# Optimization experiments

Hardware: AMD Instinct MI355X
Metric: run time of the kernel (lower is better)

The kernel has to match this reference:

```python
import jax, jax.numpy as jnp
import numpy as np

INFTY_APPROX = 1e30
LAM = 10000.0


def sinusoid_embs(length, width):
    # Transformer-XL sinusoidal embeddings, flipped so row 0 encodes the
    # largest relative distance (length-1), matching the rel_shift convention.
    pos = jnp.arange(length, dtype=jnp.float32)
    inv_lams = 1.0 / (LAM ** (jnp.arange(0, width, 2, dtype=jnp.float32) / width))
    pre = pos[:, None] * inv_lams[None, :]                 # [T, width//2]
    cat = jnp.concatenate([jnp.sin(pre), jnp.cos(pre)], axis=-1)  # [T, width]
    return jnp.flip(cat, axis=0)


def rel_shift(x):
    # x: [B, T, T] -> out[b,i,j] = x[b, i, j - i + T - 1] (XL pad/reshape trick)
    b, t, _ = x.shape
    x = jnp.pad(x, ((0, 0), (0, 0), (1, 0)))               # [B, T, T+1]
    x = x.reshape(b, t + 1, t)[:, 1:, :]                   # [B, T, T]
    return x


def setup_inputs() -> dict:
    B, T, D, K, V = 2, 4096, 1024, 128, 2048
    key = jax.random.key(0)
    ks = jax.random.split(key, 10)
    s_d = 1.0 / np.sqrt(D)
    s_v = 1.0 / np.sqrt(V)
    return {
        'x':    jax.random.normal(ks[0], (B, T, D), dtype=jnp.float32),
        'g_ln': jnp.ones((D,), dtype=jnp.float32),
        'W_q':  s_d * jax.random.normal(ks[1], (D, K), dtype=jnp.float32),
        'W_k':  s_d * jax.random.normal(ks[2], (D, K), dtype=jnp.float32),
        'W_v':  s_d * jax.random.normal(ks[3], (D, V), dtype=jnp.float32),
        'W_g':  s_d * jax.random.normal(ks[4], (D, V), dtype=jnp.float32),
        'W_r':  s_d * jax.random.normal(ks[5], (D, K), dtype=jnp.float32),
        'xl_u': 0.02 * jax.random.normal(ks[6], (K,), dtype=jnp.float32),
        'xl_v': 0.02 * jax.random.normal(ks[7], (K,), dtype=jnp.float32),
        'W_o':  s_v * jax.random.normal(ks[8], (V, D), dtype=jnp.float32),
    }


def reference(x, g_ln, W_q, W_k, W_v, W_g, W_r, xl_u, xl_v, W_o):
    B, T, D = x.shape
    K = W_q.shape[-1]
    tau = jnp.asarray(K, x.dtype) ** 0.5

    # RMSNorm input layernorm
    x_tilde = x * jax.lax.rsqrt(jnp.mean(jnp.square(x), axis=-1, keepdims=True) + 1e-6)
    x_tilde = x_tilde * g_ln

    # QKVG projections; queries pre-scaled by 1/tau (producer-side scaling)
    q = (x_tilde @ W_q) / tau                              # [B, T, K]
    k = x_tilde @ W_k                                      # [B, T, K]
    v = x_tilde @ W_v                                      # [B, T, V]

    # XL relative-position bias inputs
    xl_r = sinusoid_embs(T, D) @ W_r                       # [T, K]

    # AC term (content) and BD term (position) with XL u/v biases
    scores_ac = jnp.einsum('bik,bjk->bij', q + xl_u, k)    # [B, T, T]
    scores_bd = jnp.einsum('bik,jk->bij', q + xl_v, xl_r)  # [B, T, T]
    scores_bd = rel_shift(scores_bd)

    scores = scores_ac + scores_bd
    keep = jnp.tril(jnp.ones((T, T), dtype=bool))          # causal keep mask
    scores = scores - jnp.asarray(INFTY_APPROX, x.dtype) * jnp.logical_not(keep)

    w = jax.nn.softmax(scores, axis=-1)                    # [B, T, T]
    wv = jnp.einsum('bij,bjv->biv', w, v)                  # [B, T, V]

    # SHGA gating (GAU-style silu gate)
    wv = wv * jax.nn.silu(x_tilde @ W_g)

    res = wv @ W_o                                         # [B, T, D]
    return res
```

## Files before the change

kernel.cpp:

```cpp
#include <hip/hip_runtime.h>
#include <hip/hip_bf16.h>
#include <stdint.h>

typedef __attribute__((ext_vector_type(4))) float f32x4;
typedef __attribute__((ext_vector_type(8))) short s16x8;
typedef __attribute__((ext_vector_type(8))) unsigned short u16x8;
typedef __attribute__((ext_vector_type(4))) unsigned short u16x4;

static __device__ __forceinline__ float b2f(unsigned short u) {
  union { unsigned int i; float f; } v; v.i = ((unsigned int)u) << 16; return v.f;
}
static __device__ __forceinline__ unsigned short f2b(float f) {
  unsigned int x = __float_as_uint(f);
  return (unsigned short)((x + 0x7fffu + ((x >> 16) & 1u)) >> 16);
}

typedef __attribute__((address_space(1))) const void gconst_t;
typedef __attribute__((address_space(3))) void lds_t;
static __device__ __forceinline__ void gload_lds16(const void* g, void* l) {
  __builtin_amdgcn_global_load_lds((gconst_t*)g, (lds_t*)l, 16, 0, 0);
}

template<int N>
static __device__ __forceinline__ void vmwait() {
  asm volatile("s_waitcnt vmcnt(%0)" :: "n"(N) : "memory");
}
static __device__ __forceinline__ void barmid() {
  __builtin_amdgcn_sched_barrier(0);
  __builtin_amdgcn_s_barrier();
  asm volatile("s_waitcnt lgkmcnt(0)" ::: "memory");
  __builtin_amdgcn_sched_barrier(0);
}
static __device__ __forceinline__ void barend() {
  __builtin_amdgcn_sched_barrier(0);
  __builtin_amdgcn_s_barrier();
}

struct GemmP {
  const unsigned short* A; const unsigned short* B; void* C;
  long sA, sB, sC;
  int M, N, K, lda, ldb, ldc;
  int causal, kend_mode, swapxy;
  int gxs, gys, qchunk;
  const float* uvec; const float* vvec;
  unsigned short* qv_out; unsigned short* kk_out; float invtau;
  const float* rinv; const unsigned short* gate;
  const unsigned short* bds; float* stats;
};

template<int EPI>
__launch_bounds__(512, 2)
__global__ void gemm8p256_k(GemmP p) {
  __shared__ unsigned short L[2][4][8192];
  const int lin = (int)blockIdx.x + (int)gridDim.x * ((int)blockIdx.y + (int)gridDim.y * (int)blockIdx.z);
  const int wg = (lin & 7) * p.qchunk + (lin >> 3);
  const int xx = wg & ((1 << p.gxs) - 1);
  const int yy = (wg >> p.gxs) & ((1 << p.gys) - 1);
  const int ii = p.swapxy ? yy : xx;
  const int jj = p.swapxy ? xx : yy;
  const int i0 = ii * 256, j0 = jj * 256;
  const unsigned short* Ag = p.A + (long)i0 * p.lda;
  const unsigned short* Bg = p.B + (long)j0 * p.ldb;
  const int lda = p.lda, ldb = p.ldb;
  const int NI = p.K >> 7;

  const int tid = threadIdx.x;
  const int w = tid >> 6, l = tid & 63;
  const int wr = w >> 2, wc = w & 3;
  const int fr = l & 15, fq = l >> 4;

  auto stA = [&](int slot, int h, int t) {
#pragma unroll
    for (int u = 0; u < 2; ++u) {
      const int sl = u * 512 + tid, r = sl >> 3, g = sl & 7;
      const int gs = g ^ (r & 7);
      gload_lds16(Ag + (long)(h * 128 + r) * lda + t * 64 + gs * 8, &L[slot][h][sl * 8]);
    }
  };
  auto stB = [&](int slot, int h, int t) {
#pragma unroll
    for (int u = 0; u < 2; ++u) {
      const int sl = u * 512 + tid, r = sl >> 3, g = sl & 7;
      const int gs = g ^ (r & 7);
      gload_lds16(Bg + (long)(h * 128 + r) * ldb + t * 64 + gs * 8, &L[slot][2 + h][sl * 8]);
    }
  };

  f32x4 acc[8][4];
#pragma unroll
  for (int m = 0; m < 8; ++m)
#pragma unroll
    for (int n = 0; n < 4; ++n) acc[m][n] = (f32x4){0.f, 0.f, 0.f, 0.f};

  const int sx = (fr & 7) << 4;
  const int abase = ((fr << 7) + (fq << 4)) ^ sx;
  const int bbase = (((wc & 1) << 13) + (fr << 7) + (fq << 4)) ^ sx;
  s16x8 a[4][2], bA[2][2], bB[2][2];

  auto rdA = [&](int slot, int mq) {
#pragma unroll
    for (int m = 0; m < 4; ++m)
#pragma unroll
      for (int ks = 0; ks < 2; ++ks)
        a[m][ks] = *(const s16x8*)((const char*)&L[slot][wr][0] +
                                   ((abase ^ (ks << 6)) | ((mq * 4 + m) << 11)));
  };
  auto rdB = [&](int slot, int nq, s16x8 (&bb)[2][2]) {
    const int reg = 2 + (wc >> 1);
#pragma unroll
    for (int n = 0; n < 2; ++n)
#pragma unroll
      for (int ks = 0; ks < 2; ++ks)
        bb[n][ks] = *(const s16x8*)((const char*)&L[slot][reg][0] +
                                    ((bbase ^ (ks << 6)) | ((nq * 2 + n) << 11)));
  };
  auto mm = [&](int mq, int nq, s16x8 (&bb)[2][2]) {
    __builtin_amdgcn_s_setprio(1);
#pragma unroll
    for (int m = 0; m < 4; ++m)
#pragma unroll
      for (int n = 0; n < 2; ++n)
#pragma unroll
        for (int ks = 0; ks < 2; ++ks)
          acc[mq * 4 + m][nq * 2 + n] =
              __builtin_amdgcn_mfma_f32_16x16x32_bf16(a[m][ks], bb[n][ks],
                                                      acc[mq * 4 + m][nq * 2 + n], 0, 0, 0);
    __builtin_amdgcn_s_setprio(0);
  };

  stB(0, 0, 0); stB(0, 1, 0); stA(0, 0, 0); stA(0, 1, 0);
  stB(1, 0, 1); stB(1, 1, 1);
  vmwait<4>();
  barend();

  for (int it = 0; it < NI; ++it) {
    const int t0 = 2 * it, t1 = t0 + 1;
    const bool lastI = (it == NI - 1);
    rdA(0, 0); rdB(0, 0, bA); stA(1, 0, t1);
    barmid(); mm(0, 0, bA); barend();
    rdB(0, 1, bB); stA(1, 1, t1);
    barmid(); mm(0, 1, bB); barend();
    rdA(0, 1);
    if (!lastI) stB(0, 0, t0 + 2);
    barmid(); mm(1, 1, bB); barend();
    if (!lastI) stB(0, 1, t0 + 2);
    barmid(); mm(1, 0, bA);
    if (lastI) vmwait<0>(); else vmwait<4>();
    barend();
    rdA(1, 0); rdB(1, 0, bA);
    if (!lastI) stA(0, 0, t0 + 2);
    barmid(); mm(0, 0, bA); barend();
    rdB(1, 1, bB);
    if (!lastI) stA(0, 1, t0 + 2);
    barmid(); mm(0, 1, bB); barend();
    rdA(1, 1);
    if (!lastI) stB(1, 0, t1 + 2);
    barmid(); mm(1, 1, bB); barend();
    if (!lastI) stB(1, 1, t1 + 2);
    barmid(); mm(1, 0, bA);
    if (!lastI) vmwait<4>();
    barend();
  }

  const int rb = i0 + wr * 128 + fq * 4;
  const int cb = j0 + wc * 64 + fr;
#pragma unroll
  for (int m = 0; m < 8; ++m)
#pragma unroll
    for (int n = 0; n < 4; ++n) {
      const int col = cb + n * 16;
#pragma unroll
      for (int e = 0; e < 4; ++e) {
        const int row = rb + m * 16 + e;
        const float val = acc[m][n][e];
        if constexpr (EPI == 0)
          ((unsigned short*)p.C)[(long)row * p.ldc + col] = f2b(val);
        else
          ((unsigned short*)p.C)[(long)row * p.ldc + col] = f2b(val / (1.f + __expf(-val)));
      }
    }
}

template<int PAIR, int EPI>
__launch_bounds__(512, 2)
__global__ void gemm8p128_k(GemmP p) {
  __shared__ unsigned short L[3][3][8192];
  const int lin = (int)blockIdx.x + (int)gridDim.x * ((int)blockIdx.y + (int)gridDim.y * (int)blockIdx.z);
  const int wg = (lin & 7) * p.qchunk + (lin >> 3);
  const int xx = wg & ((1 << p.gxs) - 1);
  const int yy = (wg >> p.gxs) & ((1 << p.gys) - 1);
  const int b  = wg >> (p.gxs + p.gys);
  const int jj = PAIR ? yy : (p.swapxy ? xx : yy);
  const int j0 = jj * 128;
  const unsigned short* Bg0 = p.B + (long)b * p.sB + (long)j0 * p.ldb;
  const int lda = p.lda, ldb = p.ldb;

  const int tid = threadIdx.x;
  const int w = tid >> 6, l = tid & 63;
  const int wr = w >> 1, wc = w & 1;
  const int fr = l & 15, fq = l >> 4;

  const int sx = (fr & 7) << 4;
  const int abase = ((((wr & 1) << 13) + (fr << 7) + (fq << 4))) ^ sx;
  const int bbase = (((wc << 13) + (fr << 7) + (fq << 4))) ^ sx;

  const int passes = PAIR ? 2 : 1;
  for (int ps = 0; ps < passes; ++ps) {
    const int ii = PAIR ? (ps ? xx : (15 - xx)) : (p.swapxy ? yy : xx);
    const int i0 = ii * 256;
    const unsigned short* Ag = p.A + (long)b * p.sA + (long)i0 * lda;
    const int kend = p.kend_mode ? min(p.K, i0 + 256) : p.K;
    const int NT = kend >> 6;

    auto stA = [&](int slot, int h, int t) {
#pragma unroll
      for (int u = 0; u < 2; ++u) {
        const int sl = u * 512 + tid, r = sl >> 3, g = sl & 7;
        const int gs = g ^ (r & 7);
        gload_lds16(Ag + (long)(h * 128 + r) * lda + t * 64 + gs * 8, &L[slot][h][sl * 8]);
      }
    };
    auto stB = [&](int slot, int bh, int t) {
      const int r = tid >> 3, g = tid & 7;
      const int rloc = bh * 64 + r;
      const int gs = g ^ (rloc & 7);
      gload_lds16(Bg0 + (long)rloc * ldb + t * 64 + gs * 8, &L[slot][2][bh * 4096 + tid * 8]);
    };

    f32x4 acc[4][4];
#pragma unroll
    for (int m = 0; m < 4; ++m)
#pragma unroll
      for (int n = 0; n < 4; ++n) acc[m][n] = (f32x4){0.f, 0.f, 0.f, 0.f};
    s16x8 a[4][2], bA[2][2], bB[2][2];

    auto rdA = [&](int slot) {
      const int reg = wr >> 1;
#pragma unroll
      for (int m = 0; m < 4; ++m)
#pragma unroll
        for (int ks = 0; ks < 2; ++ks)
          a[m][ks] = *(const s16x8*)((const char*)&L[slot][reg][0] +
                                     ((abase ^ (ks << 6)) | (m << 11)));
    };
    auto rdB = [&](int slot, int nq, s16x8 (&bb)[2][2]) {
#pragma unroll
      for (int n = 0; n < 2; ++n)
#pragma unroll
        for (int ks = 0; ks < 2; ++ks)
          bb[n][ks] = *(const s16x8*)((const char*)&L[slot][2][0] +
                                      ((bbase ^ (ks << 6)) | ((nq * 2 + n) << 11)));
    };
    auto mm = [&](int nq, s16x8 (&bb)[2][2]) {
      __builtin_amdgcn_s_setprio(1);
#pragma unroll
      for (int m = 0; m < 4; ++m)
#pragma unroll
        for (int n = 0; n < 2; ++n)
#pragma unroll
          for (int ks = 0; ks < 2; ++ks)
            acc[m][nq * 2 + n] =
                __builtin_amdgcn_mfma_f32_16x16x32_bf16(a[m][ks], bb[n][ks],
                                                        acc[m][nq * 2 + n], 0, 0, 0);
      __builtin_amdgcn_s_setprio(0);
    };

    stA(0, 0, 0); stB(0, 0, 0); stA(0, 1, 0); stB(0, 1, 0);
    stA(1, 0, 1); stB(1, 0, 1); stA(1, 1, 1); stB(1, 1, 1);
    vmwait<6>();
    barend();

    int s = 0;
    for (int t = 0; t < NT; ++t) {
      int s2 = s + 2; if (s2 >= 3) s2 -= 3;
      const bool pf = (t + 2 < NT);
      rdA(s); rdB(s, 0, bA);
      if (pf) { stA(s2, 0, t + 2); stB(s2, 0, t + 2); }
      barmid(); mm(0, bA); barend();
      rdB(s, 1, bB);
      if (pf) { stA(s2, 1, t + 2); stB(s2, 1, t + 2); }
      barmid(); mm(1, bB);
      if (t == NT - 2) vmwait<0>(); else if (t < NT - 2) vmwait<6>();
      barend();
      s = (s + 1 == 3) ? 0 : s + 1;
    }

    const int rb = i0 + wr * 64 + fq * 4;
    const int cb = j0 + wc * 64 + fr;
    const long tb = (long)b * p.sC;
#pragma unroll
    for (int m = 0; m < 4; ++m)
#pragma unroll
      for (int n = 0; n < 4; ++n) {
        const int col = cb + n * 16;
#pragma unroll
        for (int e = 0; e < 4; ++e) {
          const int row = rb + m * 16 + e;
          const float val = acc[m][n][e];
          if constexpr (EPI == 1) {
            ((float*)p.C)[tb + (long)row * p.ldc + col] = val;
          } else {
            const long coff = tb + (long)row * p.ldc + col;
            const float g = b2f(p.gate[coff]);
            const float r = p.rinv[b * p.M + row];
            ((unsigned short*)p.C)[coff] = f2b(val * r * g);
          }
        }
      }
  }
}

template<int NREP, int EPI>
__launch_bounds__(512, 4)
__global__ void gemm2p_k(GemmP p) {
  constexpr int BN = NREP * 64;
  constexpr int CB = NREP / 2;
  constexpr int LPT = 1 + CB;
  const int lin = (int)blockIdx.x + (((int)blockIdx.y + (int)blockIdx.z * (int)gridDim.y) << p.gxs);
  const int wg = (lin & 7) * p.qchunk + (lin >> 3);
  const int ii = wg & ((1 << p.gxs) - 1);
  const int jj = (wg >> p.gxs) & ((1 << p.gys) - 1);
  const int b  = wg >> (p.gxs + p.gys);
  const int i0 = ii * 128, j0 = jj * BN;
  if (p.causal && j0 > i0 + 127) return;
  const unsigned short* Ag = p.A + (long)b * p.sA + (long)i0 * p.lda;
  const unsigned short* Bg = p.B + (long)b * p.sB + (long)j0 * p.ldb;
  const int NT = p.K >> 5;

  __shared__ unsigned short As[3][128 * 32];
  __shared__ unsigned short Bs[3][BN * 32];

  const int tid = threadIdx.x;
  const int w = tid >> 6, l = tid & 63;
  const int wr = w >> 2, wc = w & 3;
  const int lrow = l >> 2;
  const int swz = ((l & 3) ^ ((l >> 3) & 3)) * 8;

  auto stage = [&](int t, int bi) {
    gload_lds16(Ag + (long)(w * 16 + lrow) * p.lda + t * 32 + swz, &As[bi][w * 512]);
#pragma unroll
    for (int i = 0; i < CB; ++i) {
      const int c = w * CB + i;
      gload_lds16(Bg + (long)(c * 16 + lrow) * p.ldb + t * 32 + swz, &Bs[bi][c * 512]);
    }
  };

  f32x4 acc[4][NREP];
#pragma unroll
  for (int m = 0; m < 4; ++m)
#pragma unroll
    for (int n = 0; n < NREP; ++n) acc[m][n] = (f32x4){0.f, 0.f, 0.f, 0.f};

  const int fr = l & 15, fq = l >> 4;
  const int rg = (fq ^ ((fr >> 1) & 3)) * 8;
  const int aoff = (wr * 64 + fr) * 32 + rg;
  const int boff = (wc * (NREP * 16) + fr) * 32 + rg;

  stage(0, 0);
  if (NT > 1) stage(1, 1);

  int bi = 0;
  for (int t = 0; t < NT; ++t) {
    if (t == NT - 1) vmwait<0>(); else vmwait<LPT>();
    __builtin_amdgcn_s_barrier();
    __builtin_amdgcn_sched_barrier(0);
    const unsigned short* as = &As[bi][0];
    const unsigned short* bs = &Bs[bi][0];
    s16x8 af[4], bf[NREP];
#pragma unroll
    for (int m = 0; m < 4; ++m) af[m] = *(const s16x8*)(as + aoff + m * 512);
#pragma unroll
    for (int n = 0; n < NREP; ++n) bf[n] = *(const s16x8*)(bs + boff + n * 512);
    if (t + 2 < NT) {
      int bi2 = bi + 2; if (bi2 >= 3) bi2 -= 3;
      stage(t + 2, bi2);
    }
    __builtin_amdgcn_s_setprio(1);
#pragma unroll
    for (int m = 0; m < 4; ++m)
#pragma unroll
      for (int n = 0; n < NREP; ++n)
        acc[m][n] = __builtin_amdgcn_mfma_f32_16x16x32_bf16(af[m], bf[n], acc[m][n], 0, 0, 0);
    __builtin_amdgcn_s_setprio(0);
    bi = (bi + 1 == 3) ? 0 : bi + 1;
  }

  const int rbase = i0 + wr * 64 + fq * 4;
  const int cbase = j0 + wc * (NREP * 16) + fr;
  const long tb = (long)b * p.sC;

  if constexpr (EPI == 6) {
    float psum[16];
#pragma unroll
    for (int t = 0; t < 16; ++t) psum[t] = 0.f;
#pragma unroll
    for (int m = 0; m < 4; ++m)
#pragma unroll
      for (int n = 0; n < NREP; ++n) {
        const int col = cbase + n * 16;
#pragma unroll
        for (int e = 0; e < 4; ++e) {
          const int row = rbase + m * 16 + e;
          const long o = tb + (long)row * p.ldc + col;
          float ev = 0.f;
          if (col <= row) {
            const float s = acc[m][n][e] + b2f(p.bds[o]);
            ev = __expf(fminf(s, 60.f));
          }
          ((unsigned short*)p.C)[o] = f2b(ev);
          psum[m * 4 + e] += ev;
        }
      }
#pragma unroll
    for (int t = 0; t < 16; ++t) {
      float v = psum[t];
      v += __shfl_xor(v, 1); v += __shfl_xor(v, 2);
      v += __shfl_xor(v, 4); v += __shfl_xor(v, 8);
      psum[t] = v;
    }
    if (fr == 0) {
#pragma unroll
      for (int t = 0; t < 16; ++t) {
        const int row = rbase + (t >> 2) * 16 + (t & 3);
        p.stats[((long)(b * p.M + row) * 16 + jj) * 4 + wc] = psum[t];
      }
    }
    return;
  }

#pragma unroll
  for (int m = 0; m < 4; ++m)
#pragma unroll
    for (int n = 0; n < NREP; ++n) {
      const int col = cbase + n * 16;
#pragma unroll
      for (int e = 0; e < 4; ++e) {
        const int row = rbase + m * 16 + e;
        if constexpr (EPI == 5) {
          if (col <= row)
            ((unsigned short*)p.C)[tb + (long)row * p.ldc + (row - col)] = f2b(acc[m][n][e]);
        }
      }
    }
}

template<int EPI>
__launch_bounds__(256)
__global__ void gemm_bt_k(GemmP p) {
  const int i0 = blockIdx.x * 128;
  const int j0 = blockIdx.y * 128;
  const unsigned short* A = p.A + (long)i0 * p.lda;
  const unsigned short* B = p.B + (long)j0 * p.ldb;

  __shared__ unsigned short As[128 * 32];
  __shared__ unsigned short Bs[128 * 32];

  const int tid = threadIdx.x;
  const int w = tid >> 6, l = tid & 63;
  const int wr = w >> 1, wc = w & 1;

  f32x4 acc[4][4];
#pragma unroll
  for (int m = 0; m < 4; ++m)
#pragma unroll
    for (int n = 0; n < 4; ++n) acc[m][n] = (f32x4){0.f, 0.f, 0.f, 0.f};

  const int srow = (l >> 2);
  const int scol = ((l & 3) ^ ((l >> 3) & 3)) * 8;
  const unsigned short* ga0 = A + (long)(w * 16 + srow) * p.lda + scol;
  const unsigned short* ga1 = A + (long)((w + 4) * 16 + srow) * p.lda + scol;
  const unsigned short* gb0 = B + (long)(w * 16 + srow) * p.ldb + scol;
  const unsigned short* gb1 = B + (long)((w + 4) * 16 + srow) * p.ldb + scol;
  unsigned short* la0 = As + w * 512;
  unsigned short* la1 = As + (w + 4) * 512;
  unsigned short* lb0 = Bs + w * 512;
  unsigned short* lb1 = Bs + (w + 4) * 512;

  const int rg = ((l >> 4) ^ (((l & 15) >> 1) & 3)) * 8;
  const unsigned short* ap = As + ((wr * 64) + (l & 15)) * 32 + rg;
  const unsigned short* bp = Bs + ((wc * 64) + (l & 15)) * 32 + rg;

  for (int k0 = 0; k0 < p.K; k0 += 32) {
    gload_lds16(ga0 + k0, la0);
    gload_lds16(ga1 + k0, la1);
    gload_lds16(gb0 + k0, lb0);
    gload_lds16(gb1 + k0, lb1);
    __syncthreads();
    s16x8 af[4], bfr[4];
#pragma unroll
    for (int m = 0; m < 4; ++m) af[m] = *(const s16x8*)(ap + m * 16 * 32);
#pragma unroll
    for (int n = 0; n < 4; ++n) bfr[n] = *(const s16x8*)(bp + n * 16 * 32);
#pragma unroll
    for (int m = 0; m < 4; ++m)
#pragma unroll
      for (int n = 0; n < 4; ++n)
        acc[m][n] = __builtin_amdgcn_mfma_f32_16x16x32_bf16(af[m], bfr[n], acc[m][n], 0, 0, 0);
    __syncthreads();
  }

  const int rbase = i0 + wr * 64 + (l >> 4) * 4;
  const int cbase = j0 + wc * 64 + (l & 15);
#pragma unroll
  for (int m = 0; m < 4; ++m)
#pragma unroll
    for (int n = 0; n < 4; ++n) {
      const int col = cbase + n * 16;
#pragma unroll
      for (int e = 0; e < 4; ++e) {
        const int row = rbase + m * 16 + e;
        const float val = acc[m][n][e];
        if constexpr (EPI == 0) {
          ((unsigned short*)p.C)[(long)row * p.ldc + col] = f2b(val);
        } else if constexpr (EPI == 3) {
          if (j0 == 0) {
            const float q = val * p.invtau;
            const long o = (long)row * 128 + col;
            ((unsigned short*)p.C)[o] = f2b(q + p.uvec[col]);
            p.qv_out[o] = f2b(q + p.vvec[col]);
          } else {
            p.kk_out[(long)row * 128 + (col - 128)] = f2b(val);
          }
        }
      }
    }
}

__launch_bounds__(256)
__global__ void rmsnorm_k(const float* __restrict__ x, const float* __restrict__ g,
                          unsigned short* __restrict__ xt) {
  const long row = blockIdx.x;
  const float* xr = x + row * 1024;
  const int t = threadIdx.x;
  const float4 v = ((const float4*)xr)[t];
  float ss = v.x * v.x + v.y * v.y + v.z * v.z + v.w * v.w;
#pragma unroll
  for (int o = 1; o < 64; o <<= 1) ss += __shfl_xor(ss, o);
  __shared__ float wsum[4];
  if ((t & 63) == 0) wsum[t >> 6] = ss;
  __syncthreads();
  const float tot = wsum[0] + wsum[1] + wsum[2] + wsum[3];
  const float r = 1.0f / sqrtf(tot * (1.0f / 1024.0f) + 1e-6f);
  const float4 gv = ((const float4*)g)[t];
  u16x4 o;
  o.x = f2b(v.x * r * gv.x); o.y = f2b(v.y * r * gv.y);
  o.z = f2b(v.z * r * gv.z); o.w = f2b(v.w * r * gv.w);
  ((u16x4*)(xt + row * 1024))[t] = o;
}

__launch_bounds__(256)
__global__ void sinemb_k(unsigned short* __restrict__ emb) {
  const int idx = blockIdx.x * 256 + threadIdx.x;
  const int t = idx >> 10, w = idx & 1023;
  const int h = w & 511;
  const float inv = __expf(-(float)h * (9.2103403719761836f / 512.0f));
  const float pre = (float)t * inv;
  const float val = (w < 512) ? sinf(pre) : cosf(pre);
  emb[idx] = f2b(val);
}

__launch_bounds__(256)
__global__ void transcast_k(const float* __restrict__ in, unsigned short* __restrict__ out,
                            int R, int C) {
  __shared__ float tile[32][33];
  const int c0 = blockIdx.x * 32, r0 = blockIdx.y * 32;
  const int tx = threadIdx.x & 31, ty = threadIdx.x >> 5;
#pragma unroll
  for (int k = 0; k < 4; ++k)
    tile[ty + k * 8][tx] = in[(long)(r0 + ty + k * 8) * C + c0 + tx];
  __syncthreads();
#pragma unroll
  for (int k = 0; k < 4; ++k)
    out[(long)(c0 + ty + k * 8) * R + r0 + tx] = f2b(tile[tx][ty + k * 8]);
}

__global__ void rowinv_k(const float* __restrict__ stats, float* __restrict__ rinv,
                         int T, int BT) {
  const int idx = blockIdx.x * 256 + threadIdx.x;
  if (idx >= BT) return;
  const int i = idx & (T - 1);
  const int nt = (i >> 8) + 1;
  const float* st = stats + (long)idx * 64;
  float s = 0.f;
  for (int jt = 0; jt < nt; ++jt)
    s += st[jt * 4] + st[jt * 4 + 1] + st[jt * 4 + 2] + st[jt * 4 + 3];
  rinv[idx] = 1.0f / s;
}

extern "C" void kernel_launch(void* const* d_in, const int* in_sizes, int n_in,
                              void* d_out, int out_size, void* d_ws, size_t ws_size,
                              hipStream_t stream) {
  const float* x    = (const float*)d_in[0];
  const float* g_ln = (const float*)d_in[1];
  const float* W_q  = (const float*)d_in[2];
  const float* W_k  = (const float*)d_in[3];
  const float* W_v  = (const float*)d_in[4];
  const float* W_g  = (const float*)d_in[5];
  const float* W_r  = (const float*)d_in[6];
  const float* xl_u = (const float*)d_in[7];
  const float* xl_v = (const float*)d_in[8];
  const float* W_o  = (const float*)d_in[9];
  float* out = (float*)d_out;

  const int B = 2, T = 4096, D = 1024, K = 128, V = 2048;
  const int BT = B * T;

  char* ws = (char*)d_ws;
  size_t off = 0;
  auto alloc = [&](size_t bytes) -> void* {
    void* p = ws + off; off += (bytes + 255) & ~(size_t)255; return p;
  };
  unsigned short* XT   = (unsigned short*)alloc((size_t)BT * D * 2);
  unsigned short* WQKT = (unsigned short*)alloc((size_t)256 * D * 2);
  unsigned short* WVT  = (unsigned short*)alloc((size_t)V * D * 2);
  unsigned short* WGT  = (unsigned short*)alloc((size_t)V * D * 2);
  unsigned short* WRT  = (unsigned short*)alloc((size_t)K * D * 2);
  unsigned short* WOT  = (unsigned short*)alloc((size_t)D * V * 2);
  unsigned short* QU   = (unsigned short*)alloc((size_t)BT * K * 2);
  unsigned short* QV   = (unsigned short*)alloc((size_t)BT * K * 2);
  unsigned short* KKb  = (unsigned short*)alloc((size_t)BT * K * 2);
  unsigned short* RR   = (unsigned short*)alloc((size_t)T * K * 2);
  unsigned short* VVT  = (unsigned short*)alloc((size_t)V * BT * 2);
  unsigned short* GATE = (unsigned short*)alloc((size_t)BT * V * 2);
  float* STATS         = (float*)alloc((size_t)BT * 64 * 4);
  float* RINV          = (float*)alloc((size_t)BT * 4);
  unsigned short* EBUF = (unsigned short*)alloc((size_t)B * T * T * 2);
  unsigned short* BD2  = (unsigned short*)alloc((size_t)B * T * T * 2);
  unsigned short* EMB  = BD2;
  unsigned short* WVG  = BD2;
  if (off > ws_size) return;
  (void)in_sizes; (void)n_in; (void)out_size;

  const float invtau = 0.08838834764831845f;

  transcast_k<<<dim3(K / 32, D / 32), 256, 0, stream>>>(W_q, WQKT, D, K);
  transcast_k<<<dim3(K / 32, D / 32), 256, 0, stream>>>(W_k, WQKT + (size_t)K * D, D, K);
  transcast_k<<<dim3(V / 32, D / 32), 256, 0, stream>>>(W_v, WVT, D, V);
  transcast_k<<<dim3(V / 32, D / 32), 256, 0, stream>>>(W_g, WGT, D, V);
  transcast_k<<<dim3(K / 32, D / 32), 256, 0, stream>>>(W_r, WRT, D, K);
  transcast_k<<<dim3(D / 32, V / 32), 256, 0, stream>>>(W_o, WOT, V, D);
  rmsnorm_k<<<BT, 256, 0, stream>>>(x, g_ln, XT);
  sinemb_k<<<(T * D) / 256, 256, 0, stream>>>(EMB);

  {
    GemmP p{}; p.A = XT; p.B = WQKT; p.C = QU;
    p.M = BT; p.N = 256; p.K = D; p.lda = D; p.ldb = D; p.ldc = K;
    p.uvec = xl_u; p.vvec = xl_v; p.qv_out = QV; p.kk_out = KKb; p.invtau = invtau;
    gemm_bt_k<3><<<dim3(BT / 128, 2, 1), 256, 0, stream>>>(p);
  }
  {
    GemmP p{}; p.A = EMB; p.B = WRT; p.C = RR;
    p.M = T; p.N = K; p.K = D; p.lda = D; p.ldb = D; p.ldc = K;
    gemm_bt_k<0><<<dim3(T / 128, 1, 1), 256, 0, stream>>>(p);
  }
  {
    GemmP p{}; p.A = WVT; p.B = XT; p.C = VVT;
    p.M = V; p.N = BT; p.K = D; p.lda = D; p.ldb = D; p.ldc = BT;
    p.gxs = 3; p.gys = 5; p.qchunk = 32; p.swapxy = 0;
    gemm8p256_k<0><<<dim3(8, 32, 1), 512, 0, stream>>>(p);
  }
  {
    GemmP p{}; p.A = XT; p.B = WGT; p.C = GATE;
    p.M = BT; p.N = V; p.K = D; p.lda = D; p.ldb = D; p.ldc = V;
    p.gxs = 3; p.gys = 5; p.qchunk = 32; p.swapxy = 1;
    gemm8p256_k<2><<<dim3(8, 32, 1), 512, 0, stream>>>(p);
  }
  {
    GemmP p{}; p.A = QV; p.B = RR; p.C = BD2;
    p.sA = (long)T * K; p.sB = 0; p.sC = (long)T * T;
    p.M = T; p.N = T; p.K = K; p.lda = K; p.ldb = K; p.ldc = T; p.causal = 1;
    p.gxs = 5; p.gys = 4; p.qchunk = 128;
    gemm2p_k<4, 5><<<dim3(32, 16, B), 512, 0, stream>>>(p);
  }
  {
    GemmP p{}; p.A = QU; p.B = KKb; p.C = EBUF;
    p.sA = (long)T * K; p.sB = (long)T * K; p.sC = (long)T * T;
    p.M = T; p.N = T; p.K = K; p.lda = K; p.ldb = K; p.ldc = T; p.causal = 1;
    p.bds = BD2; p.stats = STATS;
    p.gxs = 5; p.gys = 4; p.qchunk = 128;
    gemm2p_k<4, 6><<<dim3(32, 16, B), 512, 0, stream>>>(p);
  }
  rowinv_k<<<BT / 256, 256, 0, stream>>>(STATS, RINV, T, BT);
  {
    GemmP p{}; p.A = EBUF; p.B = VVT; p.C = WVG;
    p.sA = (long)T * T; p.sB = T; p.sC = (long)T * V;
    p.M = T; p.N = V; p.K = T; p.lda = T; p.ldb = BT; p.ldc = V;
    p.kend_mode = 1; p.rinv = RINV; p.gate = GATE;
    p.gxs = 3; p.gys = 4; p.qchunk = 32;
    gemm8p128_k<1, 4><<<dim3(8, 16, 2), 512, 0, stream>>>(p);
  }
  {
    GemmP p{}; p.A = WVG; p.B = WOT; p.C = out;
    p.M = BT; p.N = D; p.K = V; p.lda = V; p.ldb = V; p.ldc = D;
    p.gxs = 3; p.gys = 5; p.qchunk = 32; p.swapxy = 1;
    gemm8p128_k<0, 1><<<dim3(8, 32, 1), 512, 0, stream>>>(p);
  }
}
```

Measured before the change: 411.7 us.

## Replace paired 256x128 GEMM kernel with 128x256 4-wave kernel for PV and output

Swaps out the old kernel for the causal weights-times-V GEMM and the output projection. The old one used 512 threads, a 256x128 tile and paired row-block passes for causal balance. The new kernel uses 256 threads with a 128x256 tile, K-steps of 32 and a three-stage LDS pipeline with a single barrier per step. Causal load balance now comes from reversing the row-block order instead of pairing rows. This is meant to reduce barrier overhead and raise MFMA density per wave, at the cost of more accumulator registers per thread and a different grid shape.

```diff
diff --git a/kernel.cpp b/kernel.cpp
--- a/kernel.cpp
+++ b/kernel.cpp
@@ -47,6 +47,108 @@
   const float* rinv; const unsigned short* gate;
   const unsigned short* bds; float* stats;
 };
+
+template<int EPI>
+__launch_bounds__(256, 2)
+__global__ void gemmw_k(GemmP p) {
+  __shared__ unsigned short As[3][128 * 32];
+  __shared__ unsigned short Bs[3][256 * 32];
+  const int lin = (int)blockIdx.x + (int)gridDim.x * ((int)blockIdx.y + (int)gridDim.y * (int)blockIdx.z);
+  const int wg = (lin & 7) * p.qchunk + (lin >> 3);
+  int ii = wg & ((1 << p.gxs) - 1);
+  const int jj = (wg >> p.gxs) & ((1 << p.gys) - 1);
+  const int b  = wg >> (p.gxs + p.gys);
+  if (p.kend_mode) ii = (1 << p.gxs) - 1 - ii;
+  const int i0 = ii * 128, j0 = jj * 256;
+  const unsigned short* Ag = p.A + (long)b * p.sA + (long)i0 * p.lda;
+  const unsigned short* Bg = p.B + (long)b * p.sB + (long)j0 * p.ldb;
+  const int lda = p.lda, ldb = p.ldb;
+  const int kend = p.kend_mode ? min(p.K, i0 + 128) : p.K;
+  const int NT = kend >> 5;
+
+  const int tid = threadIdx.x;
+  const int wc = tid >> 6, l = tid & 63;
+  const int fr = l & 15, fq = l >> 4;
+
+  auto stage = [&](int t, int s) {
+#pragma unroll
+    for (int u = 0; u < 2; ++u) {
+      const int sl = u * 256 + tid;
+      const int r = sl >> 2, g = sl & 3;
+      const int gs = g ^ ((r >> 1) & 3);
+      gload_lds16(Ag + (long)r * lda + t * 32 + gs * 8, &As[s][sl * 8]);
+    }
+#pragma unroll
+    for (int u = 0; u < 4; ++u) {
+      const int sl = u * 256 + tid;
+      const int r = sl >> 2, g = sl & 3;
+      const int gs = g ^ ((r >> 1) & 3);
+      gload_lds16(Bg + (long)r * ldb + t * 32 + gs * 8, &Bs[s][sl * 8]);
+    }
+  };
+
+  f32x4 acc[8][4];
+#pragma unroll
+  for (int m = 0; m < 8; ++m)
+#pragma unroll
+    for (int n = 0; n < 4; ++n) acc[m][n] = (f32x4){0.f, 0.f, 0.f, 0.f};
+
+  const int rg = (fq ^ ((fr >> 1) & 3)) * 8;
+  const int aoff = fr * 32 + rg;
+  const int boff = (wc * 64 + fr) * 32 + rg;
+
+  stage(0, 0);
+  if (NT > 1) stage(1, 1);
+
+  int s = 0;
+  for (int t = 0; t < NT; ++t) {
+    if (t == NT - 1) vmwait<0>(); else vmwait<6>();
+    __builtin_amdgcn_s_barrier();
+    __builtin_amdgcn_sched_barrier(0);
+    const unsigned short* as = &As[s][0];
+    const unsigned short* bs = &Bs[s][0];
+    s16x8 a[8], bf[4];
+#pragma unroll
+    for (int m = 0; m < 8; ++m) a[m] = *(const s16x8*)(as + aoff + m * 512);
+#pragma unroll
+    for (int n = 0; n < 4; ++n) bf[n] = *(const s16x8*)(bs + boff + n * 512);
+    if (t + 2 < NT) {
+      int s2 = s + 2; if (s2 >= 3) s2 -= 3;
+      stage(t + 2, s2);
+    }
+    __builtin_amdgcn_s_setprio(1);
+#pragma unroll
+    for (int m = 0; m < 8; ++m)
+#pragma unroll
+      for (int n = 0; n < 4; ++n)
+        acc[m][n] = __builtin_amdgcn_mfma_f32_16x16x32_bf16(a[m], bf[n], acc[m][n], 0, 0, 0);
+    __builtin_amdgcn_s_setprio(0);
+    s = (s + 1 == 3) ? 0 : s + 1;
+  }
+
+  const int rb = i0 + fq * 4;
+  const int cb = j0 + wc * 64 + fr;
+  const long tb = (long)b * p.sC;
+#pragma unroll
+  for (int m = 0; m < 8; ++m)
+#pragma unroll
+    for (int n = 0; n < 4; ++n) {
+      const int col = cb + n * 16;
+#pragma unroll
+      for (int e = 0; e < 4; ++e) {
+        const int row = rb + m * 16 + e;
+        const float val = acc[m][n][e];
+        if constexpr (EPI == 1) {
+          ((float*)p.C)[tb + (long)row * p.ldc + col] = val;
+        } else {
+          const long coff = tb + (long)row * p.ldc + col;
+          const float g = b2f(p.gate[coff]);
+          const float r = p.rinv[b * p.M + row];
+          ((unsigned short*)p.C)[coff] = f2b(val * r * g);
+        }
+      }
+    }
+}
 
 template<int EPI>
 __launch_bounds__(512, 2)
@@ -181,135 +283,6 @@
     }
 }
 
-template<int PAIR, int EPI>
-__launch_bounds__(512, 2)
-__global__ void gemm8p128_k(GemmP p) {
-  __shared__ unsigned short L[3][3][8192];
-  const int lin = (int)blockIdx.x + (int)gridDim.x * ((int)blockIdx.y + (int)gridDim.y * (int)blockIdx.z);
-  const int wg = (lin & 7) * p.qchunk + (lin >> 3);
-  const int xx = wg & ((1 << p.gxs) - 1);
-  const int yy = (wg >> p.gxs) & ((1 << p.gys) - 1);
-  const int b  = wg >> (p.gxs + p.gys);
-  const int jj = PAIR ? yy : (p.swapxy ? xx : yy);
-  const int j0 = jj * 128;
-  const unsigned short* Bg0 = p.B + (long)b * p.sB + (long)j0 * p.ldb;
-  const int lda = p.lda, ldb = p.ldb;
-
-  const int tid = threadIdx.x;
-  const int w = tid >> 6, l = tid & 63;
-  const int wr = w >> 1, wc = w & 1;
-  const int fr = l & 15, fq = l >> 4;
-
-  const int sx = (fr & 7) << 4;
-  const int abase = ((((wr & 1) << 13) + (fr << 7) + (fq << 4))) ^ sx;
-  const int bbase = (((wc << 13) + (fr << 7) + (fq << 4))) ^ sx;
-
-  const int passes = PAIR ? 2 : 1;
-  for (int ps = 0; ps < passes; ++ps) {
-    const int ii = PAIR ? (ps ? xx : (15 - xx)) : (p.swapxy ? yy : xx);
-    const int i0 = ii * 256;
-    const unsigned short* Ag = p.A + (long)b * p.sA + (long)i0 * lda;
-    const int kend = p.kend_mode ? min(p.K, i0 + 256) : p.K;
-    const int NT = kend >> 6;
-
-    auto stA = [&](int slot, int h, int t) {
-#pragma unroll
-      for (int u = 0; u < 2; ++u) {
-        const int sl = u * 512 + tid, r = sl >> 3, g = sl & 7;
-        const int gs = g ^ (r & 7);
-        gload_lds16(Ag + (long)(h * 128 + r) * lda + t * 64 + gs * 8, &L[slot][h][sl * 8]);
-      }
-    };
-    auto stB = [&](int slot, int bh, int t) {
-      const int r = tid >> 3, g = tid & 7;
-      const int rloc = bh * 64 + r;
-      const int gs = g ^ (rloc & 7);
-      gload_lds16(Bg0 + (long)rloc * ldb + t * 64 + gs * 8, &L[slot][2][bh * 4096 + tid * 8]);
-    };
-
-    f32x4 acc[4][4];
-#pragma unroll
-    for (int m = 0; m < 4; ++m)
-#pragma unroll
-      for (int n = 0; n < 4; ++n) acc[m][n] = (f32x4){0.f, 0.f, 0.f, 0.f};
-    s16x8 a[4][2], bA[2][2], bB[2][2];
-
-    auto rdA = [&](int slot) {
-      const int reg = wr >> 1;
-#pragma unroll
-      for (int m = 0; m < 4; ++m)
-#pragma unroll
-        for (int ks = 0; ks < 2; ++ks)
-          a[m][ks] = *(const s16x8*)((const char*)&L[slot][reg][0] +
-                                     ((abase ^ (ks << 6)) | (m << 11)));
-    };
-    auto rdB = [&](int slot, int nq, s16x8 (&bb)[2][2]) {
-#pragma unroll
-      for (int n = 0; n < 2; ++n)
-#pragma unroll
-        for (int ks = 0; ks < 2; ++ks)
-          bb[n][ks] = *(const s16x8*)((const char*)&L[slot][2][0] +
-                                      ((bbase ^ (ks << 6)) | ((nq * 2 + n) << 11)));
-    };
-    auto mm = [&](int nq, s16x8 (&bb)[2][2]) {
-      __builtin_amdgcn_s_setprio(1);
-#pragma unroll
-      for (int m = 0; m < 4; ++m)
-#pragma unroll
-        for (int n = 0; n < 2; ++n)
-#pragma unroll
-          for (int ks = 0; ks < 2; ++ks)
-            acc[m][nq * 2 + n] =
-                __builtin_amdgcn_mfma_f32_16x16x32_bf16(a[m][ks], bb[n][ks],
-                                                        acc[m][nq * 2 + n], 0, 0, 0);
-      __builtin_amdgcn_s_setprio(0);
-    };
-
-    stA(0, 0, 0); stB(0, 0, 0); stA(0, 1, 0); stB(0, 1, 0);
-    stA(1, 0, 1); stB(1, 0, 1); stA(1, 1, 1); stB(1, 1, 1);
-    vmwait<6>();
-    barend();
-
-    int s = 0;
-    for (int t = 0; t < NT; ++t) {
-      int s2 = s + 2; if (s2 >= 3) s2 -= 3;
-      const bool pf = (t + 2 < NT);
-      rdA(s); rdB(s, 0, bA);
-      if (pf) { stA(s2, 0, t + 2); stB(s2, 0, t + 2); }
-      barmid(); mm(0, bA); barend();
-      rdB(s, 1, bB);
-      if (pf) { stA(s2, 1, t + 2); stB(s2, 1, t + 2); }
-      barmid(); mm(1, bB);
-      if (t == NT - 2) vmwait<0>(); else if (t < NT - 2) vmwait<6>();
-      barend();
-      s = (s + 1 == 3) ? 0 : s + 1;
-    }
-
-    const int rb = i0 + wr * 64 + fq * 4;
-    const int cb = j0 + wc * 64 + fr;
-    const long tb = (long)b * p.sC;
-#pragma unroll
-    for (int m = 0; m < 4; ++m)
-#pragma unroll
-      for (int n = 0; n < 4; ++n) {
-        const int col = cb + n * 16;
-#pragma unroll
-        for (int e = 0; e < 4; ++e) {
-          const int row = rb + m * 16 + e;
-          const float val = acc[m][n][e];
-          if constexpr (EPI == 1) {
-            ((float*)p.C)[tb + (long)row * p.ldc + col] = val;
-          } else {
-            const long coff = tb + (long)row * p.ldc + col;
-            const float g = b2f(p.gate[coff]);
-            const float r = p.rinv[b * p.M + row];
-            ((unsigned short*)p.C)[coff] = f2b(val * r * g);
-          }
-        }
-      }
-  }
-}
-
 template<int NREP, int EPI>
 __launch_bounds__(512, 4)
 __global__ void gemm2p_k(GemmP p) {
@@ -686,13 +659,13 @@
     p.sA = (long)T * T; p.sB = T; p.sC = (long)T * V;
     p.M = T; p.N = V; p.K = T; p.lda = T; p.ldb = BT; p.ldc = V;
     p.kend_mode = 1; p.rinv = RINV; p.gate = GATE;
-    p.gxs = 3; p.gys = 4; p.qchunk = 32;
-    gemm8p128_k<1, 4><<<dim3(8, 16, 2), 512, 0, stream>>>(p);
+    p.gxs = 5; p.gys = 3; p.qchunk = 64;
+    gemmw_k<4><<<dim3(32, 8, 2), 256, 0, stream>>>(p);
   }
   {
     GemmP p{}; p.A = WVG; p.B = WOT; p.C = out;
     p.M = BT; p.N = D; p.K = V; p.lda = V; p.ldb = V; p.ldc = D;
-    p.gxs = 3; p.gys = 5; p.qchunk = 32; p.swapxy = 1;
-    gemm8p128_k<0, 1><<<dim3(8, 32, 1), 512, 0, stream>>>(p);
-  }
-}
+    p.gxs = 6; p.gys = 2; p.qchunk = 32;
+    gemmw_k<1><<<dim3(64, 4, 1), 256, 0, stream>>>(p);
+  }
+}
```

After: 454.6 us. +10.4%, slower.
